# Kernel tuning notes

Measured on AMD Instinct MI355X. Metric: run time of the kernel, lower is better.

## Reference

```python
import jax, jax.numpy as jnp
import numpy as np

N, DH, DE, T, ADIM, NOBS = 1024, 32, 16, 8, 10, 64


def setup_inputs() -> dict:
    key = jax.random.key(0)
    ks = jax.random.split(key, 16)
    s = 0.1
    return {
        "obs": jax.random.normal(ks[0], (NOBS,), jnp.float32),
        "h": jax.random.normal(ks[1], (N, DH), jnp.float32) * s,
        "types": jax.random.randint(ks[2], (N,), 0, T),
        "e": jax.random.normal(ks[3], (N, N, DE), jnp.float32) * s,
        "A": jax.random.randint(ks[4], (N, N), 0, 2),
        "r": jax.random.uniform(ks[5], (1,), jnp.float32),
        "w_ih_n": jax.random.normal(ks[6], (T, 3 * DH, DE), jnp.float32) * s,
        "w_hh_n": jax.random.normal(ks[7], (T, 3 * DH, DH), jnp.float32) * s,
        "b_n": jax.random.normal(ks[8], (T, 3 * DH), jnp.float32) * s,
        "bn_n": jax.random.normal(ks[9], (T, DH), jnp.float32) * s,
        "W_out": jax.random.normal(ks[10], (DE, DH), jnp.float32) * s,
        "b_out": jax.random.normal(ks[11], (DE,), jnp.float32) * s,
        "w_ih_e": jax.random.normal(ks[12], (T, 3 * DE, 2 * DE + 1), jnp.float32) * s,
        "w_hh_e": jax.random.normal(ks[13], (T, 3 * DE, DE), jnp.float32) * s,
        "b_e": jax.random.normal(ks[14], (T, 3 * DE), jnp.float32) * s,
        "bn_e": jax.random.normal(ks[15], (T, DE), jnp.float32) * s,
    }


def _gru_from_gates(ig, hg, h, bn):
    # equinox nn.GRUCell: gates split as (reset, update, new)
    ir, iz, inn = jnp.split(ig, 3, axis=-1)
    hr, hz, hn = jnp.split(hg, 3, axis=-1)
    r = jax.nn.sigmoid(ir + hr)
    z = jax.nn.sigmoid(iz + hz)
    n = jnp.tanh(inn + r * (hn + bn))
    return n + z * (h - n)


def reference(obs, h, types, e, A, r, w_ih_n, w_hh_n, b_n, bn_n, W_out, b_out,
              w_ih_e, w_hh_e, b_e, bn_e):
    Af = A.astype(e.dtype)
    # node_output: y = relu(W_out @ h_i + b_out), vmapped over nodes -> (N, DE)
    y = jax.nn.relu(jnp.einsum('nd,ed->ne', h, W_out) + b_out)
    # m = y[:,None,:] * (e * A[...,None]); x = m.sum(1) == y_i * sum_j e_ij * A_ij
    x = y * jnp.einsum('ijd,ij->id', e, Af)
    x = x.at[:NOBS, 0].set(obs)
    # per-node GRU with type-gathered weights (input DE, hidden DH)
    ig = jnp.einsum('nij,nj->ni', w_ih_n[types], x) + b_n[types]
    hg = jnp.einsum('nij,nj->ni', w_hh_n[types], h)
    h_new = _gru_from_gates(ig, hg, h, bn_n[types])
    # edge inputs: concat(y_i, y_j, r) -> (N, N, 2*DE+1)
    yi = jnp.broadcast_to(y[:, None, :], (N, N, DE))
    yj = jnp.broadcast_to(y[None, :, :], (N, N, DE))
    rr = jnp.ones((N, N, 1), e.dtype) * r
    yiyjr = jnp.concatenate([yi, yj, rr], axis=-1)
    # edge type of (i, j) == types[i]: gather weights per row, apply to all cols
    ig_e = jnp.einsum('rij,rcj->rci', w_ih_e[types], yiyjr) + b_e[types][:, None, :]
    hg_e = jnp.einsum('rij,rcj->rci', w_hh_e[types], e)
    e_new = _gru_from_gates(ig_e, hg_e, e, bn_e[types][:, None, :])
    a = jnp.argmax(y[-ADIM:, 0])
    return (a, h_new, e_new)
```

## Files before the change

kernel.cpp:

```cpp
#include <hip/hip_runtime.h>
#include <math.h>

#define NN 1024
#define DHH 32
#define DEE 16
#define TT 8
#define NOBS_ 64
#define ADIM_ 10
#define NSPLIT 2

typedef _Float16 h4 __attribute__((ext_vector_type(4)));
typedef float f4 __attribute__((ext_vector_type(4)));

__device__ __forceinline__ float rcp_(float x) { return __builtin_amdgcn_rcpf(x); }
__device__ __forceinline__ float sig_(float x) { return rcp_(1.0f + __expf(-x)); }
__device__ __forceinline__ float tanh_(float x) { return 1.0f - 2.0f * rcp_(1.0f + __expf(2.0f * x)); }

__global__ __launch_bounds__(256) void y_kernel(const float* __restrict__ h,
                                                const float* __restrict__ W_out,
                                                const float* __restrict__ b_out,
                                                float* __restrict__ y,
                                                _Float16* __restrict__ y_h) {
  int gid = blockIdx.x * 256 + threadIdx.x;
  int i = gid >> 4, d = gid & 15;
  const float* hp = h + i * DHH;
  const float* wp = W_out + d * DHH;
  float s = b_out[d];
#pragma unroll
  for (int q = 0; q < DHH; ++q) s = fmaf(hp[q], wp[q], s);
  s = fmaxf(s, 0.0f);
  y[gid] = s;
  y_h[gid] = (_Float16)s;
}

__global__ __launch_bounds__(256) void prep_kernel(const float* __restrict__ y,
                                                   const int* __restrict__ types,
                                                   const float* __restrict__ w_ih_e,
                                                   const float* __restrict__ b_e,
                                                   const float* __restrict__ rs,
                                                   float* __restrict__ base) {
  int gid = blockIdx.x * 256 + threadIdx.x;
  int i = gid / 48, k = gid - (gid / 48) * 48;
  int t = types[i];
  const float* w = w_ih_e + (t * 48 + k) * 33;
  const float* yp = y + i * DEE;
  float s = b_e[t * 48 + k] + rs[0] * w[32];
#pragma unroll
  for (int q = 0; q < DEE; ++q) s = fmaf(w[q], yp[q], s);
  base[gid] = s;
}

__global__ __launch_bounds__(256, 4) void edge_kernel(
    const float* __restrict__ e, const int* __restrict__ A,
    const float* __restrict__ w_hh_e, const float* __restrict__ w_ih_e,
    const float* __restrict__ bn_e, const int* __restrict__ types,
    const float* __restrict__ base, const _Float16* __restrict__ yh,
    float* __restrict__ e_new, float* __restrict__ rowsum_part) {
  __shared__ float red[4][16];
  const int b = blockIdx.x;
  const int i = b >> 1;
  const int s = b & 1;
  const int tid = threadIdx.x;
  const int lane = tid & 63, wid = tid >> 6;
  const int lj = lane & 15;
  const int kg = lane >> 4;
  const int t = types[i];

  const float* Wt = w_hh_e + t * 768;
  h4 ar, az, an;
  {
    f4 vr = *(const f4*)(Wt + lj * 16 + kg * 4);
    f4 vz = *(const f4*)(Wt + (16 + lj) * 16 + kg * 4);
    f4 vn = *(const f4*)(Wt + (32 + lj) * 16 + kg * 4);
#pragma unroll
    for (int q = 0; q < 4; ++q) {
      ar[q] = (_Float16)vr[q]; az[q] = (_Float16)vz[q]; an[q] = (_Float16)vn[q];
    }
  }
  const float* W2 = w_ih_e + t * 48 * 33 + 16;
  h4 cr, cz, cn;
#pragma unroll
  for (int q = 0; q < 4; ++q) {
    cr[q] = (_Float16)W2[lj * 33 + kg * 4 + q];
    cz[q] = (_Float16)W2[(16 + lj) * 33 + kg * 4 + q];
    cn[q] = (_Float16)W2[(32 + lj) * 33 + kg * 4 + q];
  }

  const f4 bsr = *(const f4*)(base + i * 48 + kg * 4);
  const f4 bsz = *(const f4*)(base + i * 48 + 16 + kg * 4);
  const f4 bsn = *(const f4*)(base + i * 48 + 32 + kg * 4);
  const f4 bnv = *(const f4*)(bn_e + t * 16 + kg * 4);

  const int jb = s * 512 + wid * 128 + lj;
  const int erow = i * NN;
  f4 acc = {0.0f, 0.0f, 0.0f, 0.0f};
  const f4 zero = {0.0f, 0.0f, 0.0f, 0.0f};

  f4 evs[8]; h4 yvs[8]; float as[8];
#pragma unroll
  for (int tt = 0; tt < 8; ++tt) {
    const int j = jb + tt * 16;
    evs[tt] = *(const f4*)(e + (erow + j) * 16 + kg * 4);
    yvs[tt] = *(const h4*)(yh + j * 16 + kg * 4);
    as[tt] = (float)A[erow + j];
  }

#pragma unroll
  for (int tt = 0; tt < 8; ++tt) {
    const f4 ev = evs[tt];
    const h4 yv = yvs[tt];
    const float aij = as[tt];

    h4 bf;
#pragma unroll
    for (int q = 0; q < 4; ++q) bf[q] = (_Float16)ev[q];

    f4 dr = __builtin_amdgcn_mfma_f32_16x16x16f16(ar, bf, zero, 0, 0, 0);
    f4 dz = __builtin_amdgcn_mfma_f32_16x16x16f16(az, bf, zero, 0, 0, 0);
    f4 dh = __builtin_amdgcn_mfma_f32_16x16x16f16(an, bf, zero, 0, 0, 0);
    dr = __builtin_amdgcn_mfma_f32_16x16x16f16(cr, yv, dr, 0, 0, 0);
    dz = __builtin_amdgcn_mfma_f32_16x16x16f16(cz, yv, dz, 0, 0, 0);
    const f4 di = __builtin_amdgcn_mfma_f32_16x16x16f16(cn, yv, zero, 0, 0, 0);

#pragma unroll
    for (int q = 0; q < 4; ++q) acc[q] = fmaf(ev[q], aij, acc[q]);

    float* op = e_new + (erow + jb + tt * 16) * 16 + kg * 4;
#pragma unroll
    for (int q = 0; q < 4; ++q) {
      const float rg = sig_(bsr[q] + dr[q]);
      const float zg = sig_(bsz[q] + dz[q]);
      const float ng = tanh_(bsn[q] + di[q] + rg * (dh[q] + bnv[q]));
      op[q] = ng + zg * (ev[q] - ng);
    }
  }

#pragma unroll
  for (int m = 1; m <= 8; m <<= 1) {
#pragma unroll
    for (int q = 0; q < 4; ++q) acc[q] += __shfl_xor(acc[q], m, 64);
  }
  if (lj == 0) {
#pragma unroll
    for (int q = 0; q < 4; ++q) red[wid][kg * 4 + q] = acc[q];
  }
  __syncthreads();
  if (tid < 16)
    rowsum_part[(i * NSPLIT + s) * 16 + tid] =
        red[0][tid] + red[1][tid] + red[2][tid] + red[3][tid];
}

__global__ __launch_bounds__(256) void node_kernel(
    const float* __restrict__ obs, const float* __restrict__ h,
    const int* __restrict__ types, const float* __restrict__ w_ih_n,
    const float* __restrict__ w_hh_n, const float* __restrict__ b_n,
    const float* __restrict__ bn_n, const float* __restrict__ y,
    const float* __restrict__ rowsum_part, float* __restrict__ out) {
  const int tid = threadIdx.x;
  const int node = blockIdx.x * 8 + (tid >> 5);
  const int d = tid & 31;
  const int t = types[node];
  float x[16];
#pragma unroll
  for (int q = 0; q < 16; ++q) {
    const float* rp = rowsum_part + node * NSPLIT * 16 + q;
    float rs = rp[0] + rp[16];
    x[q] = y[node * 16 + q] * rs;
  }
  if (node < NOBS_) x[0] = obs[node];
  const float* wi = w_ih_n + t * 96 * 16;
  const float* wh = w_hh_n + t * 96 * 32;
  const float* hp = h + node * 32;
  float ir = b_n[t * 96 + d], iz = b_n[t * 96 + 32 + d], in_ = b_n[t * 96 + 64 + d];
#pragma unroll
  for (int q = 0; q < 16; ++q) {
    ir = fmaf(wi[d * 16 + q], x[q], ir);
    iz = fmaf(wi[(32 + d) * 16 + q], x[q], iz);
    in_ = fmaf(wi[(64 + d) * 16 + q], x[q], in_);
  }
  float hr = 0.0f, hz = 0.0f, hn = 0.0f;
#pragma unroll
  for (int q = 0; q < 32; ++q) {
    hr = fmaf(wh[d * 32 + q], hp[q], hr);
    hz = fmaf(wh[(32 + d) * 32 + q], hp[q], hz);
    hn = fmaf(wh[(64 + d) * 32 + q], hp[q], hn);
  }
  float rg = sig_(ir + hr), zg = sig_(iz + hz);
  float ng = tanh_(in_ + rg * (hn + bn_n[t * 32 + d]));
  out[1 + node * 32 + d] = ng + zg * (hp[d] - ng);

  if (blockIdx.x == 0 && tid == 0) {
    int bi = 0;
    float best = y[(NN - ADIM_) * 16];
    for (int l = 1; l < ADIM_; ++l) {
      float v = y[(NN - ADIM_ + l) * 16];
      if (v > best) { best = v; bi = l; }
    }
    out[0] = (float)bi;
  }
}

extern "C" void kernel_launch(void* const* d_in, const int* in_sizes, int n_in,
                              void* d_out, int out_size, void* d_ws, size_t ws_size,
                              hipStream_t stream) {
  const float* obs   = (const float*)d_in[0];
  const float* h     = (const float*)d_in[1];
  const int*   types = (const int*)d_in[2];
  const float* e     = (const float*)d_in[3];
  const int*   A     = (const int*)d_in[4];
  const float* r     = (const float*)d_in[5];
  const float* w_ih_n = (const float*)d_in[6];
  const float* w_hh_n = (const float*)d_in[7];
  const float* b_n    = (const float*)d_in[8];
  const float* bn_n   = (const float*)d_in[9];
  const float* W_out  = (const float*)d_in[10];
  const float* b_out  = (const float*)d_in[11];
  const float* w_ih_e = (const float*)d_in[12];
  const float* w_hh_e = (const float*)d_in[13];
  const float* b_e    = (const float*)d_in[14];
  const float* bn_e   = (const float*)d_in[15];

  float* ws = (float*)d_ws;
  float* y_buf       = ws;
  float* base        = y_buf + 16384;
  float* rowsum_part = base + 49152;
  _Float16* y_h      = (_Float16*)(rowsum_part + 32768);

  float* out   = (float*)d_out;
  float* out_e = out + 1 + NN * DHH;

  y_kernel<<<64, 256, 0, stream>>>(h, W_out, b_out, y_buf, y_h);
  prep_kernel<<<192, 256, 0, stream>>>(y_buf, types, w_ih_e, b_e, r, base);
  edge_kernel<<<NN * NSPLIT, 256, 0, stream>>>(e, A, w_hh_e, w_ih_e, bn_e, types,
                                               base, y_h, out_e, rowsum_part);
  node_kernel<<<128, 256, 0, stream>>>(obs, h, types, w_ih_n, w_hh_n, b_n, bn_n,
                                       y_buf, rowsum_part, out);
}
```

Before: 42.78 us.

## Pre-convert edge GRU weights to fp16 in prep and split edge rows four ways

The prep kernel now also converts w_hh_e and the y_j slice of w_ih_e to fp16 tables, so each edge block loads ready-made h4 weight fragments instead of strided fp32 loads and per-block conversion. The edge kernel splits each row into four blocks of 256 columns, which doubles the grid and halves the per-thread register buffers. Edge and y loads are also issued before the weight loads to overlap latency. The cost is more blocks, each doing repeated setup, plus a larger rowsum partial buffer for the node kernel to sum.

```diff
diff --git a/kernel.cpp b/kernel.cpp
--- a/kernel.cpp
+++ b/kernel.cpp
@@ -7,7 +7,7 @@
 #define TT 8
 #define NOBS_ 64
 #define ADIM_ 10
-#define NSPLIT 2
+#define NSPLIT 4
 
 typedef _Float16 h4 __attribute__((ext_vector_type(4)));
 typedef float f4 __attribute__((ext_vector_type(4)));
@@ -36,77 +36,77 @@
 __global__ __launch_bounds__(256) void prep_kernel(const float* __restrict__ y,
                                                    const int* __restrict__ types,
                                                    const float* __restrict__ w_ih_e,
+                                                   const float* __restrict__ w_hh_e,
                                                    const float* __restrict__ b_e,
                                                    const float* __restrict__ rs,
-                                                   float* __restrict__ base) {
+                                                   float* __restrict__ base,
+                                                   _Float16* __restrict__ w16hh,
+                                                   _Float16* __restrict__ w16ih) {
   int gid = blockIdx.x * 256 + threadIdx.x;
-  int i = gid / 48, k = gid - (gid / 48) * 48;
-  int t = types[i];
-  const float* w = w_ih_e + (t * 48 + k) * 33;
-  const float* yp = y + i * DEE;
-  float s = b_e[t * 48 + k] + rs[0] * w[32];
-#pragma unroll
-  for (int q = 0; q < DEE; ++q) s = fmaf(w[q], yp[q], s);
-  base[gid] = s;
+  if (gid < NN * 48) {
+    int i = gid / 48, k = gid - (gid / 48) * 48;
+    int t = types[i];
+    const float* w = w_ih_e + (t * 48 + k) * 33;
+    const float* yp = y + i * DEE;
+    float s = b_e[t * 48 + k] + rs[0] * w[32];
+#pragma unroll
+    for (int q = 0; q < DEE; ++q) s = fmaf(w[q], yp[q], s);
+    base[gid] = s;
+  } else {
+    int u = gid - NN * 48;
+    if (u < TT * 48 * 16) {
+      w16hh[u] = (_Float16)w_hh_e[u];
+    } else {
+      int v = u - TT * 48 * 16;
+      int row = v >> 4, k = v & 15;
+      w16ih[v] = (_Float16)w_ih_e[row * 33 + 16 + k];
+    }
+  }
 }
 
 __global__ __launch_bounds__(256, 4) void edge_kernel(
     const float* __restrict__ e, const int* __restrict__ A,
-    const float* __restrict__ w_hh_e, const float* __restrict__ w_ih_e,
+    const _Float16* __restrict__ w16hh, const _Float16* __restrict__ w16ih,
     const float* __restrict__ bn_e, const int* __restrict__ types,
     const float* __restrict__ base, const _Float16* __restrict__ yh,
     float* __restrict__ e_new, float* __restrict__ rowsum_part) {
   __shared__ float red[4][16];
   const int b = blockIdx.x;
-  const int i = b >> 1;
-  const int s = b & 1;
+  const int i = b >> 2;
+  const int s = b & 3;
   const int tid = threadIdx.x;
   const int lane = tid & 63, wid = tid >> 6;
   const int lj = lane & 15;
   const int kg = lane >> 4;
+  const int jb = s * 256 + wid * 64 + lj;
+  const int erow = i * NN;
+
+  f4 evs[4]; h4 yvs[4]; float as[4];
+#pragma unroll
+  for (int tt = 0; tt < 4; ++tt) {
+    const int j = jb + tt * 16;
+    evs[tt] = *(const f4*)(e + (erow + j) * 16 + kg * 4);
+    yvs[tt] = *(const h4*)(yh + j * 16 + kg * 4);
+    as[tt] = (float)A[erow + j];
+  }
+
   const int t = types[i];
-
-  const float* Wt = w_hh_e + t * 768;
-  h4 ar, az, an;
-  {
-    f4 vr = *(const f4*)(Wt + lj * 16 + kg * 4);
-    f4 vz = *(const f4*)(Wt + (16 + lj) * 16 + kg * 4);
-    f4 vn = *(const f4*)(Wt + (32 + lj) * 16 + kg * 4);
-#pragma unroll
-    for (int q = 0; q < 4; ++q) {
-      ar[q] = (_Float16)vr[q]; az[q] = (_Float16)vz[q]; an[q] = (_Float16)vn[q];
-    }
-  }
-  const float* W2 = w_ih_e + t * 48 * 33 + 16;
-  h4 cr, cz, cn;
-#pragma unroll
-  for (int q = 0; q < 4; ++q) {
-    cr[q] = (_Float16)W2[lj * 33 + kg * 4 + q];
-    cz[q] = (_Float16)W2[(16 + lj) * 33 + kg * 4 + q];
-    cn[q] = (_Float16)W2[(32 + lj) * 33 + kg * 4 + q];
-  }
-
+  const h4 ar = *(const h4*)(w16hh + (t * 48 + lj) * 16 + kg * 4);
+  const h4 az = *(const h4*)(w16hh + (t * 48 + 16 + lj) * 16 + kg * 4);
+  const h4 an = *(const h4*)(w16hh + (t * 48 + 32 + lj) * 16 + kg * 4);
+  const h4 cr = *(const h4*)(w16ih + (t * 48 + lj) * 16 + kg * 4);
+  const h4 cz = *(const h4*)(w16ih + (t * 48 + 16 + lj) * 16 + kg * 4);
+  const h4 cn = *(const h4*)(w16ih + (t * 48 + 32 + lj) * 16 + kg * 4);
   const f4 bsr = *(const f4*)(base + i * 48 + kg * 4);
   const f4 bsz = *(const f4*)(base + i * 48 + 16 + kg * 4);
   const f4 bsn = *(const f4*)(base + i * 48 + 32 + kg * 4);
   const f4 bnv = *(const f4*)(bn_e + t * 16 + kg * 4);
 
-  const int jb = s * 512 + wid * 128 + lj;
-  const int erow = i * NN;
   f4 acc = {0.0f, 0.0f, 0.0f, 0.0f};
   const f4 zero = {0.0f, 0.0f, 0.0f, 0.0f};
 
-  f4 evs[8]; h4 yvs[8]; float as[8];
-#pragma unroll
-  for (int tt = 0; tt < 8; ++tt) {
-    const int j = jb + tt * 16;
-    evs[tt] = *(const f4*)(e + (erow + j) * 16 + kg * 4);
-    yvs[tt] = *(const h4*)(yh + j * 16 + kg * 4);
-    as[tt] = (float)A[erow + j];
-  }
-
-#pragma unroll
-  for (int tt = 0; tt < 8; ++tt) {
+#pragma unroll
+  for (int tt = 0; tt < 4; ++tt) {
     const f4 ev = evs[tt];
     const h4 yv = yvs[tt];
     const float aij = as[tt];
@@ -164,7 +164,7 @@
 #pragma unroll
   for (int q = 0; q < 16; ++q) {
     const float* rp = rowsum_part + node * NSPLIT * 16 + q;
-    float rs = rp[0] + rp[16];
+    float rs = rp[0] + rp[16] + rp[32] + rp[48];
     x[q] = y[node * 16 + q] * rs;
   }
   if (node < NOBS_) x[0] = obs[node];
@@ -224,14 +224,17 @@
   float* y_buf       = ws;
   float* base        = y_buf + 16384;
   float* rowsum_part = base + 49152;
-  _Float16* y_h      = (_Float16*)(rowsum_part + 32768);
+  _Float16* y_h      = (_Float16*)(rowsum_part + 65536);
+  _Float16* w16hh    = y_h + 16384;
+  _Float16* w16ih    = w16hh + 6144;
 
   float* out   = (float*)d_out;
   float* out_e = out + 1 + NN * DHH;
 
   y_kernel<<<64, 256, 0, stream>>>(h, W_out, b_out, y_buf, y_h);
-  prep_kernel<<<192, 256, 0, stream>>>(y_buf, types, w_ih_e, b_e, r, base);
-  edge_kernel<<<NN * NSPLIT, 256, 0, stream>>>(e, A, w_hh_e, w_ih_e, bn_e, types,
+  prep_kernel<<<240, 256, 0, stream>>>(y_buf, types, w_ih_e, w_hh_e, b_e, r,
+                                       base, w16hh, w16ih);
+  edge_kernel<<<NN * NSPLIT, 256, 0, stream>>>(e, A, w16hh, w16ih, bn_e, types,
                                                base, y_h, out_e, rowsum_part);
   node_kernel<<<128, 256, 0, stream>>>(obs, h, types, w_ih_n, w_hh_n, b_n, bn_n,
                                        y_buf, rowsum_part, out);
```

New measurement: 43.43 us. About the same (+1.5%).
